# Kernel optimization log

Hardware: AMD Instinct MI355X
Metric: run time of the kernel (lower is better)

## Reference

```python
import jax, jax.numpy as jnp
import numpy as np

N = 100000       # nodes per graph
H = 384          # hidden_dim
GRID = 10 * 10 * 7   # flattened grid feature size (10x10 UV grid, 7 channels)
NTYPES = 6       # len(surface_type_map)
ENT = NTYPES + 1 # one-hot entity_types + scalar area


def setup_inputs() -> dict:
    key = jax.random.key(0)
    ks = jax.random.split(key, 16)
    f32 = jnp.float32
    d = {}
    d["x1"] = jax.random.normal(ks[0], (N, 10, 10, 7), dtype=f32)
    d["is_face1"] = jax.random.uniform(ks[1], (N,), dtype=f32)
    d["entity_types1"] = jax.random.randint(ks[2], (N,), 0, NTYPES)
    d["area1"] = jax.random.uniform(ks[3], (N,), dtype=f32)
    d["x2"] = jax.random.normal(ks[4], (N, 10, 10, 7), dtype=f32)
    d["is_face2"] = jax.random.uniform(ks[5], (N,), dtype=f32)
    d["entity_types2"] = jax.random.randint(ks[6], (N,), 0, NTYPES)
    d["area2"] = jax.random.uniform(ks[7], (N,), dtype=f32)
    # MLP params (num_layers=2: Linear -> ELU -> Linear), fan-in scaled init
    d["W1g"] = jax.random.normal(ks[8], (GRID, H), dtype=f32) / np.sqrt(GRID)
    d["b1g"] = jnp.zeros((H,), dtype=f32)
    d["W2g"] = jax.random.normal(ks[9], (H, H), dtype=f32) / np.sqrt(H)
    d["b2g"] = jnp.zeros((H,), dtype=f32)
    d["W1e"] = jax.random.normal(ks[10], (ENT, H), dtype=f32) / np.sqrt(ENT)
    d["b1e"] = jnp.zeros((H,), dtype=f32)
    d["W2e"] = jax.random.normal(ks[11], (H, H), dtype=f32) / np.sqrt(H)
    d["b2e"] = jnp.zeros((H,), dtype=f32)
    return d


def _embed_one(x, is_face, entity_types, area, W1g, b1g, W2g, b2g, W1e, b1e, W2e, b2e):
    n = x.shape[0]
    face_mask = is_face > 0.5                      # which nodes are B-rep faces
    grid = x.reshape(n, -1)                        # [n, 700], mlp path
    hg = jax.nn.elu(grid @ W1g + b1g) @ W2g + b2g  # grid branch MLP
    ent = jnp.concatenate(
        [jax.nn.one_hot(entity_types, NTYPES, dtype=x.dtype), area[:, None]], axis=1
    )                                              # [n, 7]
    he = jax.nn.elu(ent @ W1e + b1e) @ W2e + b2e   # entity branch MLP
    # gather->MLP->scatter-add into zeros == masked dense (no batchnorm, row-wise MLP)
    return jnp.where(face_mask[:, None], hg + he, jnp.zeros((), x.dtype))


def reference(x1, is_face1, entity_types1, area1, x2, is_face2, entity_types2, area2,
              W1g, b1g, W2g, b2g, W1e, b1e, W2e, b2e):
    o1 = _embed_one(x1, is_face1, entity_types1, area1, W1g, b1g, W2g, b2g, W1e, b1e, W2e, b2e)
    o2 = _embed_one(x2, is_face2, entity_types2, area2, W1g, b1g, W2g, b2g, W1e, b1e, W2e, b2e)
    return (o1, o2)
```

## Files before the change

kernel.cpp:

```cpp
#include <hip/hip_runtime.h>
#include <hip/hip_bf16.h>

typedef __attribute__((ext_vector_type(8))) short short8;
typedef __attribute__((ext_vector_type(4))) short svec4;
typedef __attribute__((ext_vector_type(8))) __bf16 bf16x8;
typedef __attribute__((ext_vector_type(4))) float f32x4;

#define NN 100000
#define HD 384
#define K1T 22
#define K2T 24
#define NBLK 98

#define OFF_B1  0
#define OFF_B2  540672
#define OFF_T   1130496
#define OFF_V   1139712
#define OFF_BI  1141248
#define OFF_IDX 1142784
#define OFF_CNT 1942784
#define OFF_OFFS 1943568
#define OFF_TOT 1944352

union Frag { short s[8]; bf16x8 v; };

__device__ __forceinline__ short f2bf(float f) {
  union { __bf16 h; short s; } u;
  u.h = (__bf16)f;
  return u.s;
}

__device__ __forceinline__ float elu(float v) {
  return v > 0.f ? v : __expf(v) - 1.f;
}

__global__ void prep_kernel(const float* __restrict__ W1g, const float* __restrict__ b1g,
                            const float* __restrict__ W2g, const float* __restrict__ b2g,
                            const float* __restrict__ W1e, const float* __restrict__ b1e,
                            const float* __restrict__ W2e, const float* __restrict__ b2e,
                            char* __restrict__ ws) {
  int t = blockIdx.x * 256 + threadIdx.x;
  short* B1 = (short*)(ws + OFF_B1);
  short* B2 = (short*)(ws + OFF_B2);
  float* Tt = (float*)(ws + OFF_T);
  float* Vt = (float*)(ws + OFF_V);
  float* Bi = (float*)(ws + OFF_BI);
  if (t < 33792) {
    int lane = t & 63, rest = t >> 6;
    int kt = rest % K1T, nt = rest / K1T;
    int col = nt * 16 + (lane & 15);
    int kb = kt * 32 + (lane >> 4) * 8;
    short8 v;
#pragma unroll
    for (int i = 0; i < 8; ++i) {
      int k = kb + i;
      v[i] = (k < 700) ? f2bf(W1g[k * 384 + col]) : (short)0;
    }
    *(short8*)(B1 + (size_t)t * 8) = v;
  } else if (t < 70656) {
    int t2 = t - 33792;
    int lane = t2 & 63, rest = t2 >> 6;
    int kt = rest % K2T, nt = rest / K2T;
    int col = nt * 16 + (lane & 15);
    int kb = kt * 32 + (lane >> 4) * 8;
    short8 v;
#pragma unroll
    for (int i = 0; i < 8; ++i) {
      int k = kb + i;
      v[i] = (k < 384) ? f2bf(W2g[k * 384 + col]) : f2bf(W2e[(k - 384) * 384 + col]);
    }
    *(short8*)(B2 + (size_t)t2 * 8) = v;
  } else if (t < 73728) {
    int r = t - 70656;
    int which = r / 384, c = r % 384;
    if (which < 6)       Tt[r] = W1e[which * 384 + c] + b1e[c];
    else if (which == 6) Vt[c] = W1e[6 * 384 + c];
    else                 Bi[c] = b2g[c] + b2e[c];
  }
}

__global__ void count_kernel(const float* __restrict__ isf1, const float* __restrict__ isf2,
                             char* __restrict__ ws) {
  int g = blockIdx.y;
  const float* isf = g ? isf2 : isf1;
  int i = blockIdx.x * 1024 + threadIdx.x;
  bool face = (i < NN) && (isf[i] > 0.5f);
  unsigned long long b = __ballot(face);
  __shared__ int wc[16];
  int lane = threadIdx.x & 63, wid = threadIdx.x >> 6;
  if (lane == 0) wc[wid] = __popcll(b);
  __syncthreads();
  if (threadIdx.x == 0) {
    int s = 0;
#pragma unroll
    for (int w = 0; w < 16; ++w) s += wc[w];
    ((int*)(ws + OFF_CNT))[g * NBLK + blockIdx.x] = s;
  }
}

__global__ void scan_kernel(char* __restrict__ ws) {
  int t = threadIdx.x;
  if (t < 2) {
    const int* cnt = (const int*)(ws + OFF_CNT) + t * NBLK;
    int* offs = (int*)(ws + OFF_OFFS) + t * NBLK;
    int* tot = (int*)(ws + OFF_TOT);
    int run = 0;
    for (int b = 0; b < NBLK; ++b) { offs[b] = run; run += cnt[b]; }
    tot[t] = run;
  }
}

__global__ void compact_kernel(const float* __restrict__ isf1, const float* __restrict__ isf2,
                               char* __restrict__ ws) {
  int g = blockIdx.y;
  const float* isf = g ? isf2 : isf1;
  const int* offs = (const int*)(ws + OFF_OFFS) + g * NBLK;
  int totF = ((const int*)(ws + OFF_TOT))[g];
  int* idx = (int*)(ws + OFF_IDX) + g * NN;
  int bx = blockIdx.x;
  int i = bx * 1024 + threadIdx.x;
  bool valid = i < NN;
  bool face = valid && (isf[i] > 0.5f);
  unsigned long long bf = __ballot(face);
  unsigned long long bv = __ballot(valid);
  int lane = threadIdx.x & 63, wid = threadIdx.x >> 6;
  __shared__ int wF[16], wV[16];
  if (lane == 0) { wF[wid] = __popcll(bf); wV[wid] = __popcll(bv); }
  __syncthreads();
  int baseF = 0, baseV = 0;
  for (int w = 0; w < wid; ++w) { baseF += wF[w]; baseV += wV[w]; }
  unsigned long long lmask = (1ull << lane) - 1ull;
  int pF = __popcll(bf & lmask);
  int pV = __popcll(bv & lmask);
  if (face) {
    idx[offs[bx] + baseF + pF] = i;
  } else if (valid) {
    int nfBefore = bx * 1024 - offs[bx];
    int nfIn = (baseV + pV) - (baseF + pF);
    idx[totF + nfBefore + nfIn] = i;
  }
}

__global__ __launch_bounds__(256, 3) void face_embed_kernel(
    const float* __restrict__ x1, const int* __restrict__ et1, const float* __restrict__ ar1,
    const float* __restrict__ x2, const int* __restrict__ et2, const float* __restrict__ ar2,
    const float* __restrict__ b1g, const char* __restrict__ ws,
    float* __restrict__ out) {
  const int g = blockIdx.y;
  const float* x = g ? x2 : x1;
  const int* et  = g ? et2 : et1;
  const float* ar = g ? ar2 : ar1;
  float* o = out + (size_t)g * NN * HD;
  const int* idx = (const int*)(ws + OFF_IDX) + g * NN;
  const int totF = ((const int*)(ws + OFF_TOT))[g];
  const int nFB = (totF + 31) >> 5;
  const int bx = blockIdx.x;
  const int tid = threadIdx.x;

  if (bx >= nFB) {
    int totN = NN - totF;
    int base = (bx - nFB) * 32;
    if (base >= totN) return;
    const int* idxN = idx + totF;
    f32x4 z = {0.f, 0.f, 0.f, 0.f};
#pragma unroll
    for (int it = 0; it < 12; ++it) {
      int c = tid + it * 256;
      int r = c / 96, cc = c % 96;
      if (base + r < totN) {
        int node = idxN[base + r];
        *(f32x4*)(o + (size_t)node * HD + cc * 4) = z;
      }
    }
    return;
  }

  __shared__ short As[32 * 704];
  __shared__ int sN[32];
  short* h1s = As;

  const bf16x8* B1 = (const bf16x8*)(ws + OFF_B1);
  const bf16x8* B2 = (const bf16x8*)(ws + OFF_B2);
  const float* Tg  = (const float*)(ws + OFF_T);
  const float* Vg  = (const float*)(ws + OFF_V);
  const float* Big = (const float*)(ws + OFF_BI);

  const int row0 = bx * 32;
  if (tid < 32) {
    sN[tid] = (row0 + tid < totF) ? idx[row0 + tid] : -1;
    int byte = (tid * 1408 + 1400) ^ ((tid & 7) << 4);
    *(unsigned long long*)((char*)As + byte) = 0ull;
  }
  __syncthreads();

#pragma unroll 4
  for (int it = 0; it < 22; ++it) {
    int c = tid + it * 256;
    if (c < 5600) {
      int r = c / 175, cc = c % 175;
      int node = sN[r];
      if (node >= 0) {
        f32x4 v = *(const f32x4*)(x + (size_t)node * 700 + cc * 4);
        svec4 p;
#pragma unroll
        for (int i = 0; i < 4; ++i) p[i] = f2bf(v[i]);
        int byte = (r * 1408 + cc * 8) ^ ((r & 7) << 4);
        *(svec4*)((char*)As + byte) = p;
      }
    }
  }

  const int wid = tid >> 6, lane = tid & 63;
  const int lr = lane & 15, gq = lane >> 4;

  float b1c[6], b2c[6];
#pragma unroll
  for (int n = 0; n < 6; ++n) {
    int col = (wid * 6 + n) * 16 + lr;
    b1c[n] = b1g[col];
    b2c[n] = Big[col];
  }
  __syncthreads();

  f32x4 acc[2][6] = {};
  for (int kt = 0; kt < K1T; ++kt) {
    Frag a[2];
#pragma unroll
    for (int m = 0; m < 2; ++m) {
      int row = m * 16 + lr;
      int byte = (row * 1408 + kt * 64 + gq * 16) ^ ((row & 7) << 4);
      a[m].v = *(const bf16x8*)((const char*)As + byte);
    }
#pragma unroll
    for (int n = 0; n < 6; ++n) {
      bf16x8 b = B1[((wid * 6 + n) * K1T + kt) * 64 + lane];
#pragma unroll
      for (int m = 0; m < 2; ++m)
        acc[m][n] = __builtin_amdgcn_mfma_f32_16x16x32_bf16(a[m].v, b, acc[m][n], 0, 0, 0);
    }
  }
  __syncthreads();

#pragma unroll
  for (int m = 0; m < 2; ++m)
#pragma unroll
    for (int n = 0; n < 6; ++n) {
      int col = (wid * 6 + n) * 16 + lr;
#pragma unroll
      for (int r2 = 0; r2 < 4; ++r2) {
        int row = m * 16 + 4 * gq + r2;
        float hv = elu(acc[m][n][r2] + b1c[n]);
        int byte = (row * 768 + col * 2) ^ ((row & 15) << 4);
        *(short*)((char*)h1s + byte) = f2bf(hv);
      }
    }
  __syncthreads();

  int nde[2]; float nda[2];
#pragma unroll
  for (int m = 0; m < 2; ++m) {
    int node = sN[m * 16 + lr];
    if (node >= 0) { nde[m] = et[node]; nda[m] = ar[node]; }
    else           { nde[m] = 0;        nda[m] = 0.f; }
  }

  f32x4 acc2[2][6] = {};
  for (int kt = 0; kt < K2T; ++kt) {
    Frag a[2];
    if (kt < 12) {
#pragma unroll
      for (int m = 0; m < 2; ++m) {
        int row = m * 16 + lr;
        int byte = (row * 768 + (kt * 32 + gq * 8) * 2) ^ ((row & 15) << 4);
        a[m].v = *(const bf16x8*)((const char*)h1s + byte);
      }
    } else {
      int c0 = (kt - 12) * 32 + gq * 8;
#pragma unroll
      for (int m = 0; m < 2; ++m) {
        const float* Tp = Tg + nde[m] * 384 + c0;
        const float* Vp = Vg + c0;
#pragma unroll
        for (int i = 0; i < 8; ++i)
          a[m].s[i] = f2bf(elu(Tp[i] + nda[m] * Vp[i]));
      }
    }
#pragma unroll
    for (int n = 0; n < 6; ++n) {
      bf16x8 b = B2[((wid * 6 + n) * K2T + kt) * 64 + lane];
#pragma unroll
      for (int m = 0; m < 2; ++m)
        acc2[m][n] = __builtin_amdgcn_mfma_f32_16x16x32_bf16(a[m].v, b, acc2[m][n], 0, 0, 0);
    }
  }

#pragma unroll
  for (int m = 0; m < 2; ++m) {
#pragma unroll
    for (int r2 = 0; r2 < 4; ++r2) {
      int node = sN[m * 16 + 4 * gq + r2];
      if (node >= 0) {
#pragma unroll
        for (int n = 0; n < 6; ++n) {
          int col = (wid * 6 + n) * 16 + lr;
          o[(size_t)node * HD + col] = acc2[m][n][r2] + b2c[n];
        }
      }
    }
  }
}

extern "C" void kernel_launch(void* const* d_in, const int* in_sizes, int n_in,
                              void* d_out, int out_size, void* d_ws, size_t ws_size,
                              hipStream_t stream) {
  (void)n_in; (void)out_size; (void)ws_size; (void)in_sizes;
  const float* x1  = (const float*)d_in[0];
  const float* is1 = (const float*)d_in[1];
  const int*   et1 = (const int*)d_in[2];
  const float* ar1 = (const float*)d_in[3];
  const float* x2  = (const float*)d_in[4];
  const float* is2 = (const float*)d_in[5];
  const int*   et2 = (const int*)d_in[6];
  const float* ar2 = (const float*)d_in[7];
  const float* W1g = (const float*)d_in[8];
  const float* b1g = (const float*)d_in[9];
  const float* W2g = (const float*)d_in[10];
  const float* b2g = (const float*)d_in[11];
  const float* W1e = (const float*)d_in[12];
  const float* b1e = (const float*)d_in[13];
  const float* W2e = (const float*)d_in[14];
  const float* b2e = (const float*)d_in[15];
  float* out = (float*)d_out;
  char* ws = (char*)d_ws;

  prep_kernel<<<dim3(288), dim3(256), 0, stream>>>(W1g, b1g, W2g, b2g, W1e, b1e, W2e, b2e, ws);
  count_kernel<<<dim3(NBLK, 2), dim3(1024), 0, stream>>>(is1, is2, ws);
  scan_kernel<<<dim3(1), dim3(64), 0, stream>>>(ws);
  compact_kernel<<<dim3(NBLK, 2), dim3(1024), 0, stream>>>(is1, is2, ws);

  dim3 grid(NN / 32 + 1, 2);
  face_embed_kernel<<<grid, dim3(256), 0, stream>>>(
      x1, et1, ar1, x2, et2, ar2, b1g, ws, out);
}
```

Before: 371.1 us.

## Double-buffer B fragments and precompute entity activations into LDS

Both MFMA K-loops now prefetch the next k-step's weight fragments into registers (ping-pong bP/bQ) so global B loads overlap the current MFMAs. The entity-branch hidden activations (ELU of T+area*V) are computed once cooperatively by all threads into a second LDS region, instead of being recomputed redundantly per wave inside the second GEMM loop. Shared memory grows to 48KB and register pressure rises from the extra fragments, which can reduce occupancy.

```diff
diff --git a/kernel.cpp b/kernel.cpp
--- a/kernel.cpp
+++ b/kernel.cpp
@@ -11,6 +11,7 @@
 #define K1T 22
 #define K2T 24
 #define NBLK 98
+#define HE_OFF 24576
 
 #define OFF_B1  0
 #define OFF_B2  540672
@@ -175,9 +176,10 @@
     return;
   }
 
-  __shared__ short As[32 * 704];
+  __shared__ char buf[49152];
   __shared__ int sN[32];
-  short* h1s = As;
+  char* As = buf;
+  char* h1s = buf;
 
   const bf16x8* B1 = (const bf16x8*)(ws + OFF_B1);
   const bf16x8* B2 = (const bf16x8*)(ws + OFF_B2);
@@ -189,7 +191,7 @@
   if (tid < 32) {
     sN[tid] = (row0 + tid < totF) ? idx[row0 + tid] : -1;
     int byte = (tid * 1408 + 1400) ^ ((tid & 7) << 4);
-    *(unsigned long long*)((char*)As + byte) = 0ull;
+    *(unsigned long long*)(As + byte) = 0ull;
   }
   __syncthreads();
 
@@ -205,7 +207,7 @@
 #pragma unroll
         for (int i = 0; i < 4; ++i) p[i] = f2bf(v[i]);
         int byte = (r * 1408 + cc * 8) ^ ((r & 7) << 4);
-        *(svec4*)((char*)As + byte) = p;
+        *(svec4*)(As + byte) = p;
       }
     }
   }
@@ -223,20 +225,41 @@
   __syncthreads();
 
   f32x4 acc[2][6] = {};
-  for (int kt = 0; kt < K1T; ++kt) {
-    Frag a[2];
-#pragma unroll
-    for (int m = 0; m < 2; ++m) {
-      int row = m * 16 + lr;
-      int byte = (row * 1408 + kt * 64 + gq * 16) ^ ((row & 7) << 4);
-      a[m].v = *(const bf16x8*)((const char*)As + byte);
-    }
-#pragma unroll
-    for (int n = 0; n < 6; ++n) {
-      bf16x8 b = B1[((wid * 6 + n) * K1T + kt) * 64 + lane];
-#pragma unroll
-      for (int m = 0; m < 2; ++m)
-        acc[m][n] = __builtin_amdgcn_mfma_f32_16x16x32_bf16(a[m].v, b, acc[m][n], 0, 0, 0);
+  {
+    Frag bP[6], bQ[6];
+#pragma unroll
+    for (int n = 0; n < 6; ++n) bP[n].v = B1[((wid * 6 + n) * K1T + 0) * 64 + lane];
+#pragma unroll
+    for (int kt = 0; kt < K1T; kt += 2) {
+#pragma unroll
+      for (int n = 0; n < 6; ++n) bQ[n].v = B1[((wid * 6 + n) * K1T + kt + 1) * 64 + lane];
+      Frag a[2];
+#pragma unroll
+      for (int m = 0; m < 2; ++m) {
+        int row = m * 16 + lr;
+        int byte = (row * 1408 + kt * 64 + gq * 16) ^ ((row & 7) << 4);
+        a[m].v = *(const bf16x8*)(As + byte);
+      }
+#pragma unroll
+      for (int n = 0; n < 6; ++n)
+#pragma unroll
+        for (int m = 0; m < 2; ++m)
+          acc[m][n] = __builtin_amdgcn_mfma_f32_16x16x32_bf16(a[m].v, bP[n].v, acc[m][n], 0, 0, 0);
+      if (kt + 2 < K1T) {
+#pragma unroll
+        for (int n = 0; n < 6; ++n) bP[n].v = B1[((wid * 6 + n) * K1T + kt + 2) * 64 + lane];
+      }
+#pragma unroll
+      for (int m = 0; m < 2; ++m) {
+        int row = m * 16 + lr;
+        int byte = (row * 1408 + (kt + 1) * 64 + gq * 16) ^ ((row & 7) << 4);
+        a[m].v = *(const bf16x8*)(As + byte);
+      }
+#pragma unroll
+      for (int n = 0; n < 6; ++n)
+#pragma unroll
+        for (int m = 0; m < 2; ++m)
+          acc[m][n] = __builtin_amdgcn_mfma_f32_16x16x32_bf16(a[m].v, bQ[n].v, acc[m][n], 0, 0, 0);
     }
   }
   __syncthreads();
@@ -251,46 +274,68 @@
         int row = m * 16 + 4 * gq + r2;
         float hv = elu(acc[m][n][r2] + b1c[n]);
         int byte = (row * 768 + col * 2) ^ ((row & 15) << 4);
-        *(short*)((char*)h1s + byte) = f2bf(hv);
-      }
-    }
-  __syncthreads();
-
-  int nde[2]; float nda[2];
-#pragma unroll
-  for (int m = 0; m < 2; ++m) {
-    int node = sN[m * 16 + lr];
-    if (node >= 0) { nde[m] = et[node]; nda[m] = ar[node]; }
-    else           { nde[m] = 0;        nda[m] = 0.f; }
-  }
+        *(short*)(h1s + byte) = f2bf(hv);
+      }
+    }
+  {
+    int row = tid >> 3;
+    int c0 = (tid & 7) * 48;
+    int node = sN[row];
+    int e = 0; float arv = 0.f;
+    if (node >= 0) { e = et[node]; arv = ar[node]; }
+    const float* Tp = Tg + e * 384 + c0;
+    const float* Vp = Vg + c0;
+#pragma unroll
+    for (int j = 0; j < 48; j += 2) {
+      unsigned lo = (unsigned short)f2bf(elu(Tp[j] + arv * Vp[j]));
+      unsigned hi = (unsigned short)f2bf(elu(Tp[j + 1] + arv * Vp[j + 1]));
+      int byte = HE_OFF + ((row * 768 + (c0 + j) * 2) ^ ((row & 15) << 4));
+      *(unsigned*)(buf + byte) = lo | (hi << 16);
+    }
+  }
+  __syncthreads();
 
   f32x4 acc2[2][6] = {};
-  for (int kt = 0; kt < K2T; ++kt) {
-    Frag a[2];
-    if (kt < 12) {
+  {
+    Frag bP[6], bQ[6];
+#pragma unroll
+    for (int n = 0; n < 6; ++n) bP[n].v = B2[((wid * 6 + n) * K2T + 0) * 64 + lane];
+#pragma unroll
+    for (int kt = 0; kt < K2T; kt += 2) {
+#pragma unroll
+      for (int n = 0; n < 6; ++n) bQ[n].v = B2[((wid * 6 + n) * K2T + kt + 1) * 64 + lane];
+      Frag a[2];
 #pragma unroll
       for (int m = 0; m < 2; ++m) {
         int row = m * 16 + lr;
-        int byte = (row * 768 + (kt * 32 + gq * 8) * 2) ^ ((row & 15) << 4);
-        a[m].v = *(const bf16x8*)((const char*)h1s + byte);
-      }
-    } else {
-      int c0 = (kt - 12) * 32 + gq * 8;
+        int kk = kt < 12 ? kt : kt - 12;
+        int base = kt < 12 ? 0 : HE_OFF;
+        int byte = base + ((row * 768 + kk * 64 + gq * 16) ^ ((row & 15) << 4));
+        a[m].v = *(const bf16x8*)(buf + byte);
+      }
+#pragma unroll
+      for (int n = 0; n < 6; ++n)
+#pragma unroll
+        for (int m = 0; m < 2; ++m)
+          acc2[m][n] = __builtin_amdgcn_mfma_f32_16x16x32_bf16(a[m].v, bP[n].v, acc2[m][n], 0, 0, 0);
+      if (kt + 2 < K2T) {
+#pragma unroll
+        for (int n = 0; n < 6; ++n) bP[n].v = B2[((wid * 6 + n) * K2T + kt + 2) * 64 + lane];
+      }
 #pragma unroll
       for (int m = 0; m < 2; ++m) {
-        const float* Tp = Tg + nde[m] * 384 + c0;
-        const float* Vp = Vg + c0;
-#pragma unroll
-        for (int i = 0; i < 8; ++i)
-          a[m].s[i] = f2bf(elu(Tp[i] + nda[m] * Vp[i]));
-      }
-    }
-#pragma unroll
-    for (int n = 0; n < 6; ++n) {
-      bf16x8 b = B2[((wid * 6 + n) * K2T + kt) * 64 + lane];
-#pragma unroll
-      for (int m = 0; m < 2; ++m)
-        acc2[m][n] = __builtin_amdgcn_mfma_f32_16x16x32_bf16(a[m].v, b, acc2[m][n], 0, 0, 0);
+        int row = m * 16 + lr;
+        int kt1 = kt + 1;
+        int kk = kt1 < 12 ? kt1 : kt1 - 12;
+        int base = kt1 < 12 ? 0 : HE_OFF;
+        int byte = base + ((row * 768 + kk * 64 + gq * 16) ^ ((row & 15) << 4));
+        a[m].v = *(const bf16x8*)(buf + byte);
+      }
+#pragma unroll
+      for (int n = 0; n < 6; ++n)
+#pragma unroll
+        for (int m = 0; m < 2; ++m)
+          acc2[m][n] = __builtin_amdgcn_mfma_f32_16x16x32_bf16(a[m].v, bQ[n].v, acc2[m][n], 0, 0, 0);
     }
   }
 
```

After: 361.8 us. -2.5%, faster.

## Use 64-row tiles with 512 threads and split K staging through shared memory

Applied to the files above, without the earlier changes.

The face kernel now handles 64 rows per block with 8 waves, each wave owning 48 output columns over 4 row fragments. Every B-weight fragment loaded from global memory is therefore reused across more rows. The 700-wide input is staged in two K halves through a single 48KB shared buffer to keep LDS usage bounded. The entity-branch hidden activations are computed cooperatively into shared memory instead of per-lane redundant global reads. In exchange there are extra barriers and less overlap between load and compute per block.

```diff
diff --git a/kernel.cpp b/kernel.cpp
--- a/kernel.cpp
+++ b/kernel.cpp
@@ -141,7 +141,7 @@
   }
 }
 
-__global__ __launch_bounds__(256, 3) void face_embed_kernel(
+__global__ __launch_bounds__(512, 4) void face_embed_kernel(
     const float* __restrict__ x1, const int* __restrict__ et1, const float* __restrict__ ar1,
     const float* __restrict__ x2, const int* __restrict__ et2, const float* __restrict__ ar2,
     const float* __restrict__ b1g, const char* __restrict__ ws,
@@ -153,19 +153,19 @@
   float* o = out + (size_t)g * NN * HD;
   const int* idx = (const int*)(ws + OFF_IDX) + g * NN;
   const int totF = ((const int*)(ws + OFF_TOT))[g];
-  const int nFB = (totF + 31) >> 5;
+  const int nFB = (totF + 63) >> 6;
   const int bx = blockIdx.x;
   const int tid = threadIdx.x;
 
   if (bx >= nFB) {
     int totN = NN - totF;
-    int base = (bx - nFB) * 32;
+    int base = (bx - nFB) * 64;
     if (base >= totN) return;
     const int* idxN = idx + totF;
     f32x4 z = {0.f, 0.f, 0.f, 0.f};
 #pragma unroll
     for (int it = 0; it < 12; ++it) {
-      int c = tid + it * 256;
+      int c = tid + it * 512;
       int r = c / 96, cc = c % 96;
       if (base + r < totN) {
         int node = idxN[base + r];
@@ -175,9 +175,8 @@
     return;
   }
 
-  __shared__ short As[32 * 704];
-  __shared__ int sN[32];
-  short* h1s = As;
+  __shared__ char buf[49152];
+  __shared__ int sN[64];
 
   const bf16x8* B1 = (const bf16x8*)(ws + OFF_B1);
   const bf16x8* B2 = (const bf16x8*)(ws + OFF_B2);
@@ -185,125 +184,175 @@
   const float* Vg  = (const float*)(ws + OFF_V);
   const float* Big = (const float*)(ws + OFF_BI);
 
-  const int row0 = bx * 32;
-  if (tid < 32) {
-    sN[tid] = (row0 + tid < totF) ? idx[row0 + tid] : -1;
-    int byte = (tid * 1408 + 1400) ^ ((tid & 7) << 4);
-    *(unsigned long long*)((char*)As + byte) = 0ull;
-  }
-  __syncthreads();
-
-#pragma unroll 4
-  for (int it = 0; it < 22; ++it) {
-    int c = tid + it * 256;
-    if (c < 5600) {
-      int r = c / 175, cc = c % 175;
-      int node = sN[r];
-      if (node >= 0) {
-        f32x4 v = *(const f32x4*)(x + (size_t)node * 700 + cc * 4);
-        svec4 p;
-#pragma unroll
-        for (int i = 0; i < 4; ++i) p[i] = f2bf(v[i]);
-        int byte = (r * 1408 + cc * 8) ^ ((r & 7) << 4);
-        *(svec4*)((char*)As + byte) = p;
-      }
-    }
-  }
+  const int row0 = bx * 64;
+  if (tid < 64) sN[tid] = (row0 + tid < totF) ? idx[row0 + tid] : -1;
+  __syncthreads();
 
   const int wid = tid >> 6, lane = tid & 63;
   const int lr = lane & 15, gq = lane >> 4;
 
-  float b1c[6], b2c[6];
-#pragma unroll
-  for (int n = 0; n < 6; ++n) {
-    int col = (wid * 6 + n) * 16 + lr;
+  int heRow = tid >> 3;
+  int heNode = sN[heRow];
+  int heE = 0; float heA = 0.f;
+  if (heNode >= 0) { heE = et[heNode]; heA = ar[heNode]; }
+
+  float b1c[3], b2c[3];
+#pragma unroll
+  for (int n = 0; n < 3; ++n) {
+    int col = wid * 48 + n * 16 + lr;
     b1c[n] = b1g[col];
     b2c[n] = Big[col];
   }
-  __syncthreads();
-
-  f32x4 acc[2][6] = {};
-  for (int kt = 0; kt < K1T; ++kt) {
-    Frag a[2];
-#pragma unroll
-    for (int m = 0; m < 2; ++m) {
-      int row = m * 16 + lr;
-      int byte = (row * 1408 + kt * 64 + gq * 16) ^ ((row & 7) << 4);
-      a[m].v = *(const bf16x8*)((const char*)As + byte);
-    }
-#pragma unroll
-    for (int n = 0; n < 6; ++n) {
-      bf16x8 b = B1[((wid * 6 + n) * K1T + kt) * 64 + lane];
-#pragma unroll
-      for (int m = 0; m < 2; ++m)
-        acc[m][n] = __builtin_amdgcn_mfma_f32_16x16x32_bf16(a[m].v, b, acc[m][n], 0, 0, 0);
-    }
-  }
-  __syncthreads();
-
-#pragma unroll
-  for (int m = 0; m < 2; ++m)
-#pragma unroll
-    for (int n = 0; n < 6; ++n) {
-      int col = (wid * 6 + n) * 16 + lr;
+
+  f32x4 acc[4][3] = {};
+
+#pragma unroll
+  for (int it = 0; it < 11; ++it) {
+    int c = tid + it * 512;
+    int r = c / 88, cc = c % 88;
+    int node = sN[r];
+    if (node >= 0) {
+      f32x4 v = *(const f32x4*)(x + (size_t)node * 700 + cc * 4);
+      svec4 p;
+#pragma unroll
+      for (int i = 0; i < 4; ++i) p[i] = f2bf(v[i]);
+      int byte = (r * 704 + cc * 8) ^ ((r & 7) << 4);
+      *(svec4*)(buf + byte) = p;
+    }
+  }
+  __syncthreads();
+#pragma unroll
+  for (int kt = 0; kt < 11; ++kt) {
+    Frag a[4];
+#pragma unroll
+    for (int mf = 0; mf < 4; ++mf) {
+      int row = mf * 16 + lr;
+      int byte = (row * 704 + kt * 64 + gq * 16) ^ ((row & 7) << 4);
+      a[mf].v = *(const bf16x8*)(buf + byte);
+    }
+#pragma unroll
+    for (int n = 0; n < 3; ++n) {
+      bf16x8 b = B1[((wid * 3 + n) * K1T + kt) * 64 + lane];
+#pragma unroll
+      for (int mf = 0; mf < 4; ++mf)
+        acc[mf][n] = __builtin_amdgcn_mfma_f32_16x16x32_bf16(a[mf].v, b, acc[mf][n], 0, 0, 0);
+    }
+  }
+  __syncthreads();
+
+#pragma unroll
+  for (int it = 0; it < 11; ++it) {
+    int c = tid + it * 512;
+    int r = c / 88, cc = c % 88;
+    int node = sN[r];
+    int byte = (r * 704 + cc * 8) ^ ((r & 7) << 4);
+    if (cc == 87) {
+      *(unsigned long long*)(buf + byte) = 0ull;
+    } else if (node >= 0) {
+      f32x4 v = *(const f32x4*)(x + (size_t)node * 700 + 352 + cc * 4);
+      svec4 p;
+#pragma unroll
+      for (int i = 0; i < 4; ++i) p[i] = f2bf(v[i]);
+      *(svec4*)(buf + byte) = p;
+    }
+  }
+  __syncthreads();
+#pragma unroll
+  for (int kt = 0; kt < 11; ++kt) {
+    Frag a[4];
+#pragma unroll
+    for (int mf = 0; mf < 4; ++mf) {
+      int row = mf * 16 + lr;
+      int byte = (row * 704 + kt * 64 + gq * 16) ^ ((row & 7) << 4);
+      a[mf].v = *(const bf16x8*)(buf + byte);
+    }
+#pragma unroll
+    for (int n = 0; n < 3; ++n) {
+      bf16x8 b = B1[((wid * 3 + n) * K1T + 11 + kt) * 64 + lane];
+#pragma unroll
+      for (int mf = 0; mf < 4; ++mf)
+        acc[mf][n] = __builtin_amdgcn_mfma_f32_16x16x32_bf16(a[mf].v, b, acc[mf][n], 0, 0, 0);
+    }
+  }
+  __syncthreads();
+
+#pragma unroll
+  for (int mf = 0; mf < 4; ++mf)
+#pragma unroll
+    for (int n = 0; n < 3; ++n) {
+      int col = wid * 48 + n * 16 + lr;
 #pragma unroll
       for (int r2 = 0; r2 < 4; ++r2) {
-        int row = m * 16 + 4 * gq + r2;
-        float hv = elu(acc[m][n][r2] + b1c[n]);
+        int row = mf * 16 + 4 * gq + r2;
+        float hv = elu(acc[mf][n][r2] + b1c[n]);
         int byte = (row * 768 + col * 2) ^ ((row & 15) << 4);
-        *(short*)((char*)h1s + byte) = f2bf(hv);
+        *(short*)(buf + byte) = f2bf(hv);
       }
     }
   __syncthreads();
 
-  int nde[2]; float nda[2];
-#pragma unroll
-  for (int m = 0; m < 2; ++m) {
-    int node = sN[m * 16 + lr];
-    if (node >= 0) { nde[m] = et[node]; nda[m] = ar[node]; }
-    else           { nde[m] = 0;        nda[m] = 0.f; }
-  }
-
-  f32x4 acc2[2][6] = {};
-  for (int kt = 0; kt < K2T; ++kt) {
-    Frag a[2];
-    if (kt < 12) {
-#pragma unroll
-      for (int m = 0; m < 2; ++m) {
-        int row = m * 16 + lr;
-        int byte = (row * 768 + (kt * 32 + gq * 8) * 2) ^ ((row & 15) << 4);
-        a[m].v = *(const bf16x8*)((const char*)h1s + byte);
-      }
-    } else {
-      int c0 = (kt - 12) * 32 + gq * 8;
-#pragma unroll
-      for (int m = 0; m < 2; ++m) {
-        const float* Tp = Tg + nde[m] * 384 + c0;
-        const float* Vp = Vg + c0;
-#pragma unroll
-        for (int i = 0; i < 8; ++i)
-          a[m].s[i] = f2bf(elu(Tp[i] + nda[m] * Vp[i]));
-      }
-    }
-#pragma unroll
-    for (int n = 0; n < 6; ++n) {
-      bf16x8 b = B2[((wid * 6 + n) * K2T + kt) * 64 + lane];
-#pragma unroll
-      for (int m = 0; m < 2; ++m)
-        acc2[m][n] = __builtin_amdgcn_mfma_f32_16x16x32_bf16(a[m].v, b, acc2[m][n], 0, 0, 0);
-    }
-  }
-
-#pragma unroll
-  for (int m = 0; m < 2; ++m) {
+  f32x4 acc2[4][3] = {};
+#pragma unroll
+  for (int kt = 0; kt < 12; ++kt) {
+    Frag a[4];
+#pragma unroll
+    for (int mf = 0; mf < 4; ++mf) {
+      int row = mf * 16 + lr;
+      int byte = (row * 768 + (kt * 32 + gq * 8) * 2) ^ ((row & 15) << 4);
+      a[mf].v = *(const bf16x8*)(buf + byte);
+    }
+#pragma unroll
+    for (int n = 0; n < 3; ++n) {
+      bf16x8 b = B2[((wid * 3 + n) * K2T + kt) * 64 + lane];
+#pragma unroll
+      for (int mf = 0; mf < 4; ++mf)
+        acc2[mf][n] = __builtin_amdgcn_mfma_f32_16x16x32_bf16(a[mf].v, b, acc2[mf][n], 0, 0, 0);
+    }
+  }
+  __syncthreads();
+
+  {
+    int c0 = (tid & 7) * 48;
+    const float* Tp = Tg + heE * 384 + c0;
+    const float* Vp = Vg + c0;
+#pragma unroll
+    for (int j = 0; j < 48; j += 2) {
+      unsigned lo = (unsigned short)f2bf(elu(Tp[j] + heA * Vp[j]));
+      unsigned hi = (unsigned short)f2bf(elu(Tp[j + 1] + heA * Vp[j + 1]));
+      int byte = (heRow * 768 + (c0 + j) * 2) ^ ((heRow & 15) << 4);
+      *(unsigned*)(buf + byte) = lo | (hi << 16);
+    }
+  }
+  __syncthreads();
+
+#pragma unroll
+  for (int kt = 0; kt < 12; ++kt) {
+    Frag a[4];
+#pragma unroll
+    for (int mf = 0; mf < 4; ++mf) {
+      int row = mf * 16 + lr;
+      int byte = (row * 768 + (kt * 32 + gq * 8) * 2) ^ ((row & 15) << 4);
+      a[mf].v = *(const bf16x8*)(buf + byte);
+    }
+#pragma unroll
+    for (int n = 0; n < 3; ++n) {
+      bf16x8 b = B2[((wid * 3 + n) * K2T + 12 + kt) * 64 + lane];
+#pragma unroll
+      for (int mf = 0; mf < 4; ++mf)
+        acc2[mf][n] = __builtin_amdgcn_mfma_f32_16x16x32_bf16(a[mf].v, b, acc2[mf][n], 0, 0, 0);
+    }
+  }
+
+#pragma unroll
+  for (int mf = 0; mf < 4; ++mf) {
 #pragma unroll
     for (int r2 = 0; r2 < 4; ++r2) {
-      int node = sN[m * 16 + 4 * gq + r2];
+      int node = sN[mf * 16 + 4 * gq + r2];
       if (node >= 0) {
 #pragma unroll
-        for (int n = 0; n < 6; ++n) {
-          int col = (wid * 6 + n) * 16 + lr;
-          o[(size_t)node * HD + col] = acc2[m][n][r2] + b2c[n];
+        for (int n = 0; n < 3; ++n) {
+          int col = wid * 48 + n * 16 + lr;
+          o[(size_t)node * HD + col] = acc2[mf][n][r2] + b2c[n];
         }
       }
     }
@@ -338,7 +387,7 @@
   scan_kernel<<<dim3(1), dim3(64), 0, stream>>>(ws);
   compact_kernel<<<dim3(NBLK, 2), dim3(1024), 0, stream>>>(is1, is2, ws);
 
-  dim3 grid(NN / 32 + 1, 2);
-  face_embed_kernel<<<grid, dim3(256), 0, stream>>>(
+  dim3 grid(NN / 64 + 2, 2);
+  face_embed_kernel<<<grid, dim3(512), 0, stream>>>(
       x1, et1, ar1, x2, et2, ar2, b1g, ws, out);
 }
```

Result: slower. 490.9 us (+32.3%).

## Double-buffer K-panels of grid input to overlap global loads with GEMM1

Applied to the files above, without the earlier changes.

Replaces the single 44KB LDS tile holding the full 700-wide input rows with two 12KB panels. Each panel is loaded into registers, converted to bf16 and written while the MFMA loop runs on the other panel, so global gather latency overlaps compute. The smaller LDS footprint and reuse of one accumulator array allow occupancy to rise from 3 to 6 blocks per CU. The risks are register pressure from the staging registers under the tighter launch bound, and the extra barriers between panels.

```diff
diff --git a/kernel.cpp b/kernel.cpp
--- a/kernel.cpp
+++ b/kernel.cpp
@@ -11,6 +11,7 @@
 #define K1T 22
 #define K2T 24
 #define NBLK 98
+#define PANB 12288
 
 #define OFF_B1  0
 #define OFF_B2  540672
@@ -141,7 +142,27 @@
   }
 }
 
-__global__ __launch_bounds__(256, 3) void face_embed_kernel(
+#define GEMM1_PANEL(PAN, KTBASE, NKT)                                              \
+  { const char* pan_ = (PAN);                                                      \
+    _Pragma("unroll")                                                              \
+    for (int ktL = 0; ktL < (NKT); ++ktL) {                                        \
+      Frag a_[2];                                                                  \
+      _Pragma("unroll")                                                            \
+      for (int m = 0; m < 2; ++m) {                                                \
+        int row = m * 16 + lr;                                                     \
+        int byte = (row * 384 + ktL * 64 + gq * 16) ^ ((row & 7) << 4);            \
+        a_[m].v = *(const bf16x8*)(pan_ + byte);                                   \
+      }                                                                            \
+      _Pragma("unroll")                                                            \
+      for (int n = 0; n < 6; ++n) {                                                \
+        bf16x8 b_ = B1[((wid * 6 + n) * K1T + (KTBASE) + ktL) * 64 + lane];        \
+        _Pragma("unroll")                                                          \
+        for (int m = 0; m < 2; ++m)                                                \
+          acc[m][n] = __builtin_amdgcn_mfma_f32_16x16x32_bf16(a_[m].v, b_, acc[m][n], 0, 0, 0); \
+      }                                                                            \
+    } }
+
+__global__ __launch_bounds__(256, 6) void face_embed_kernel(
     const float* __restrict__ x1, const int* __restrict__ et1, const float* __restrict__ ar1,
     const float* __restrict__ x2, const int* __restrict__ et2, const float* __restrict__ ar2,
     const float* __restrict__ b1g, const char* __restrict__ ws,
@@ -175,9 +196,8 @@
     return;
   }
 
-  __shared__ short As[32 * 704];
+  __shared__ char buf[24576];
   __shared__ int sN[32];
-  short* h1s = As;
 
   const bf16x8* B1 = (const bf16x8*)(ws + OFF_B1);
   const bf16x8* B2 = (const bf16x8*)(ws + OFF_B2);
@@ -186,29 +206,8 @@
   const float* Big = (const float*)(ws + OFF_BI);
 
   const int row0 = bx * 32;
-  if (tid < 32) {
-    sN[tid] = (row0 + tid < totF) ? idx[row0 + tid] : -1;
-    int byte = (tid * 1408 + 1400) ^ ((tid & 7) << 4);
-    *(unsigned long long*)((char*)As + byte) = 0ull;
-  }
-  __syncthreads();
-
-#pragma unroll 4
-  for (int it = 0; it < 22; ++it) {
-    int c = tid + it * 256;
-    if (c < 5600) {
-      int r = c / 175, cc = c % 175;
-      int node = sN[r];
-      if (node >= 0) {
-        f32x4 v = *(const f32x4*)(x + (size_t)node * 700 + cc * 4);
-        svec4 p;
-#pragma unroll
-        for (int i = 0; i < 4; ++i) p[i] = f2bf(v[i]);
-        int byte = (r * 1408 + cc * 8) ^ ((r & 7) << 4);
-        *(svec4*)((char*)As + byte) = p;
-      }
-    }
-  }
+  if (tid < 32) sN[tid] = (row0 + tid < totF) ? idx[row0 + tid] : -1;
+  __syncthreads();
 
   const int wid = tid >> 6, lane = tid & 63;
   const int lr = lane & 15, gq = lane >> 4;
@@ -220,25 +219,81 @@
     b1c[n] = b1g[col];
     b2c[n] = Big[col];
   }
-  __syncthreads();
+  int nde[2]; float nda[2];
+#pragma unroll
+  for (int m = 0; m < 2; ++m) {
+    int node = sN[m * 16 + lr];
+    if (node >= 0) { nde[m] = et[node]; nda[m] = ar[node]; }
+    else           { nde[m] = 0;        nda[m] = 0.f; }
+  }
+
+  f32x4 st[6];
+  auto issue6 = [&](int p) {
+#pragma unroll
+    for (int it = 0; it < 6; ++it) {
+      int c = tid + it * 256;
+      int r = c / 48, cc = c % 48;
+      int node = sN[r];
+      st[it] = (node >= 0) ? *(const f32x4*)(x + (size_t)node * 700 + p * 192 + cc * 4)
+                           : (f32x4){0.f, 0.f, 0.f, 0.f};
+    }
+  };
+  auto write6 = [&](char* pan) {
+#pragma unroll
+    for (int it = 0; it < 6; ++it) {
+      int c = tid + it * 256;
+      int r = c / 48, cc = c % 48;
+      svec4 pk;
+#pragma unroll
+      for (int i = 0; i < 4; ++i) pk[i] = f2bf(st[it][i]);
+      int byte = (r * 384 + cc * 8) ^ ((r & 7) << 4);
+      *(svec4*)(pan + byte) = pk;
+    }
+  };
+  auto issue4 = [&]() {
+#pragma unroll
+    for (int it = 0; it < 4; ++it) {
+      int c = tid + it * 256;
+      int r = c >> 5, cc = c & 31;
+      int node = sN[r];
+      st[it] = (node >= 0 && cc < 31) ? *(const f32x4*)(x + (size_t)node * 700 + 576 + cc * 4)
+                                      : (f32x4){0.f, 0.f, 0.f, 0.f};
+    }
+  };
+  auto write4 = [&](char* pan) {
+#pragma unroll
+    for (int it = 0; it < 4; ++it) {
+      int c = tid + it * 256;
+      int r = c >> 5, cc = c & 31;
+      svec4 pk;
+#pragma unroll
+      for (int i = 0; i < 4; ++i) pk[i] = f2bf(st[it][i]);
+      int byte = (r * 384 + cc * 8) ^ ((r & 7) << 4);
+      *(svec4*)(pan + byte) = pk;
+    }
+  };
 
   f32x4 acc[2][6] = {};
-  for (int kt = 0; kt < K1T; ++kt) {
-    Frag a[2];
-#pragma unroll
-    for (int m = 0; m < 2; ++m) {
-      int row = m * 16 + lr;
-      int byte = (row * 1408 + kt * 64 + gq * 16) ^ ((row & 7) << 4);
-      a[m].v = *(const bf16x8*)((const char*)As + byte);
-    }
-#pragma unroll
-    for (int n = 0; n < 6; ++n) {
-      bf16x8 b = B1[((wid * 6 + n) * K1T + kt) * 64 + lane];
-#pragma unroll
-      for (int m = 0; m < 2; ++m)
-        acc[m][n] = __builtin_amdgcn_mfma_f32_16x16x32_bf16(a[m].v, b, acc[m][n], 0, 0, 0);
-    }
-  }
+
+  issue6(0); write6(buf);
+  __syncthreads();
+
+  issue6(1);
+  GEMM1_PANEL(buf, 0, 6);
+  write6(buf + PANB);
+  __syncthreads();
+
+  issue6(2);
+  GEMM1_PANEL(buf + PANB, 6, 6);
+  write6(buf);
+  __syncthreads();
+
+  issue4();
+  GEMM1_PANEL(buf, 12, 6);
+  write4(buf + PANB);
+  __syncthreads();
+
+  GEMM1_PANEL(buf + PANB, 18, 4);
   __syncthreads();
 
 #pragma unroll
@@ -251,20 +306,17 @@
         int row = m * 16 + 4 * gq + r2;
         float hv = elu(acc[m][n][r2] + b1c[n]);
         int byte = (row * 768 + col * 2) ^ ((row & 15) << 4);
-        *(short*)((char*)h1s + byte) = f2bf(hv);
-      }
-    }
-  __syncthreads();
-
-  int nde[2]; float nda[2];
-#pragma unroll
-  for (int m = 0; m < 2; ++m) {
-    int node = sN[m * 16 + lr];
-    if (node >= 0) { nde[m] = et[node]; nda[m] = ar[node]; }
-    else           { nde[m] = 0;        nda[m] = 0.f; }
-  }
-
-  f32x4 acc2[2][6] = {};
+        *(short*)(buf + byte) = f2bf(hv);
+      }
+    }
+  __syncthreads();
+
+#pragma unroll
+  for (int m = 0; m < 2; ++m)
+#pragma unroll
+    for (int n = 0; n < 6; ++n)
+      acc[m][n] = (f32x4){0.f, 0.f, 0.f, 0.f};
+
   for (int kt = 0; kt < K2T; ++kt) {
     Frag a[2];
     if (kt < 12) {
@@ -272,7 +324,7 @@
       for (int m = 0; m < 2; ++m) {
         int row = m * 16 + lr;
         int byte = (row * 768 + (kt * 32 + gq * 8) * 2) ^ ((row & 15) << 4);
-        a[m].v = *(const bf16x8*)((const char*)h1s + byte);
+        a[m].v = *(const bf16x8*)(buf + byte);
       }
     } else {
       int c0 = (kt - 12) * 32 + gq * 8;
@@ -290,7 +342,7 @@
       bf16x8 b = B2[((wid * 6 + n) * K2T + kt) * 64 + lane];
 #pragma unroll
       for (int m = 0; m < 2; ++m)
-        acc2[m][n] = __builtin_amdgcn_mfma_f32_16x16x32_bf16(a[m].v, b, acc2[m][n], 0, 0, 0);
+        acc[m][n] = __builtin_amdgcn_mfma_f32_16x16x32_bf16(a[m].v, b, acc[m][n], 0, 0, 0);
     }
   }
 
@@ -303,7 +355,7 @@
 #pragma unroll
         for (int n = 0; n < 6; ++n) {
           int col = (wid * 6 + n) * 16 + lr;
-          o[(size_t)node * HD + col] = acc2[m][n][r2] + b2c[n];
+          o[(size_t)node * HD + col] = acc[m][n][r2] + b2c[n];
         }
       }
     }
```

Result: slower. 893.0 us (+140.6%).
